# Kernel tuning notes

Hardware: AMD Instinct MI355X
Metric: run time of the kernel (lower is better)

## Reference

```python
import jax, jax.numpy as jnp
import numpy as np
from itertools import product

# dims
V, B, C, H, Wd = 3, 4, 64, 120, 160   # views, batch, feat2d_channel, image H/W
D3 = 96                               # feat3d_dim
G = 64                                # voxel grid side
N = 200000                            # sparse voxel count
NL = 250000                           # number of link rows
K = 27                                # 3^3 sparse-conv kernel offsets
EPS = 1e-5


def _build_kernel_map(rng):
    # unique sparse coordinates (b,x,y,z) sampled from a B*G^3 grid, sorted by linear code
    lin = np.sort(rng.choice(B * G * G * G, size=N, replace=False)).astype(np.int64)
    b = lin // (G * G * G)
    r = lin % (G * G * G)
    x = r // (G * G)
    y = (r // G) % G
    z = r % G
    in_idx = np.zeros((K, N), np.int32)
    mask = np.zeros((K, N), bool)
    for k, (dx, dy, dz) in enumerate(product((-1, 0, 1), repeat=3)):
        qx, qy, qz = x + dx, y + dy, z + dz
        inb = (qx >= 0) & (qx < G) & (qy >= 0) & (qy < G) & (qz >= 0) & (qz < G)
        qc = ((b * G + np.clip(qx, 0, G - 1)) * G + np.clip(qy, 0, G - 1)) * G + np.clip(qz, 0, G - 1)
        pos = np.clip(np.searchsorted(lin, qc), 0, N - 1)
        ok = inb & (lin[pos] == qc)
        in_idx[k] = np.where(ok, pos, 0)
        mask[k] = ok
    return jnp.asarray(in_idx), jnp.asarray(mask)


def setup_inputs() -> dict:
    rng = np.random.default_rng(0)
    key = jax.random.key(0)
    ks = jax.random.split(key, 8)
    feat_2d_all = jax.random.normal(ks[0], (V, B, C, H, Wd), jnp.float32)
    feat3d_F = jax.random.normal(ks[1], (N, D3), jnp.float32)
    # links: (NL, 4, V) = [batch_idx, v(row), u(col), valid]
    links = np.stack([
        rng.integers(0, B, (NL, V)),
        rng.integers(0, H, (NL, V)),
        rng.integers(0, Wd, (NL, V)),
        rng.integers(0, 2, (NL, V)),
    ], axis=1).astype(np.int32)
    coords_map_out = rng.permutation(N).astype(np.int32)
    coords_map_in = rng.choice(NL, N, replace=False).astype(np.int32)
    in_idx, nbr_mask = _build_kernel_map(rng)
    s = 0.05
    W1 = jax.random.normal(ks[2], (K, V * C, C), jnp.float32) * s
    W2 = jax.random.normal(ks[3], (K, C, D3), jnp.float32) * s
    W3 = jax.random.normal(ks[4], (K, 2 * D3, D3), jnp.float32) * s
    return {
        'feat_2d_all': feat_2d_all, 'feat3d_F': feat3d_F,
        'links': jnp.asarray(links),
        'coords_map_in': jnp.asarray(coords_map_in),
        'coords_map_out': jnp.asarray(coords_map_out),
        'in_idx': in_idx, 'nbr_mask': nbr_mask,
        'W1': W1, 'g1': jnp.ones((C,)), 'b1': jnp.zeros((C,)),
        'W2': W2, 'g2': jnp.ones((D3,)), 'b2': jnp.zeros((D3,)),
        'W3': W3, 'g3': jnp.ones((D3,)), 'b3': jnp.zeros((D3,)),
    }


def _sconv(x, Wk, in_idx, nbr_mask):
    # sparse 3x3x3 conv: out[i] = sum_k x[nbr(i,k)] @ Wk[k], masked where no neighbor
    out = jnp.zeros((x.shape[0], Wk.shape[-1]), x.dtype)
    for k in range(Wk.shape[0]):
        g = x[in_idx[k]] * nbr_mask[k][:, None].astype(x.dtype)
        out = out + g @ Wk[k]
    return out


def _bn_relu(x, g, b):
    mu = x.mean(axis=0)
    var = x.var(axis=0)
    return jax.nn.relu(g * (x - mu) / jnp.sqrt(var + EPS) + b)


def reference(feat_2d_all, feat3d_F, links, coords_map_in, coords_map_out,
              in_idx, nbr_mask, W1, g1, b1, W2, g2, b2, W3, g3, b3):
    n = feat3d_F.shape[0]
    v_, c = feat_2d_all.shape[0], feat_2d_all.shape[2]
    # current_links[coords_map_out] = links[coords_map_in]
    cur = jnp.zeros((n, 4, v_), links.dtype).at[coords_map_out].set(links[coords_map_in])
    bi = cur[:, 0, :].T   # (V, n)
    hi = cur[:, 1, :].T
    wi = cur[:, 2, :].T
    val = cur[:, 3, :].T
    vs = jnp.arange(v_)[:, None]
    # per-view gather from (V,B,C,H,W): advanced indices around the channel slice -> (V, n, C)
    g = feat_2d_all[vs, bi, :, hi, wi]
    g = g * val[:, :, None].astype(g.dtype)
    feat_2d_to_3d = jnp.transpose(g, (1, 0, 2)).reshape(n, v_ * c)
    # view_fusion: conv3 -> BN -> ReLU -> conv3 -> BN -> ReLU
    h = _bn_relu(_sconv(feat_2d_to_3d, W1, in_idx, nbr_mask), g1, b1)
    h = _bn_relu(_sconv(h, W2, in_idx, nbr_mask), g2, b2)
    # cat with 3d features, fuse_to_3d: conv3 -> BN -> ReLU
    cat = jnp.concatenate([feat3d_F, h], axis=-1)
    out = _bn_relu(_sconv(cat, W3, in_idx, nbr_mask), g3, b3)
    return out
```

## Files before the change

kernel.cpp:

```cpp
#include <hip/hip_runtime.h>
#include <stdint.h>


constexpr int NPT = 200000;
constexpr int KNB = 27;

typedef unsigned short u16;
typedef __attribute__((ext_vector_type(8))) short     bf16x8;
typedef __attribute__((ext_vector_type(8))) unsigned short u16x8;
typedef __attribute__((ext_vector_type(16))) float    f32x16;

static __device__ __forceinline__ u16 f2bf(float f){
  unsigned int u = __float_as_uint(f);
  unsigned int r = (u + 0x7fffu + ((u >> 16) & 1u)) >> 16;
  return (u16)r;
}
static __device__ __forceinline__ float bf2f(u16 u){
  return __uint_as_float(((unsigned int)u) << 16);
}

__global__ void detect_mask_kernel(const int* __restrict__ m32, int* __restrict__ flag){
  if (threadIdx.x == 0 && blockIdx.x == 0){
    int ok = 1;
    for (int i = 0; i < 64; ++i){ int v = m32[i]; if (v != 0 && v != 1) ok = 0; }
    *flag = ok;
  }
}

__global__ __launch_bounds__(256) void transpose2d_kernel(const float* __restrict__ in,
                                                          u16* __restrict__ out){
  __shared__ float tile[64][33];
  int bid = blockIdx.x;
  int wt = bid % 5;  int rest = bid / 5;
  int h  = rest % 120; rest /= 120;
  int b  = rest % 4;  int v = rest / 4;
  int w0 = wt * 32;
  int tx = threadIdx.x & 31;
  int ty = threadIdx.x >> 5;
  const float* ip = in + ((size_t)(v*4 + b) * 64) * 19200 + h * 160 + w0;
  #pragma unroll
  for (int cc = 0; cc < 8; ++cc){
    int c = cc * 8 + ty;
    tile[c][tx] = ip[(size_t)c * 19200 + tx];
  }
  __syncthreads();
  u16* op = out + (((size_t)(v*4 + b) * 120 + h) * 160 + w0) * 64;
  int c = threadIdx.x & 63;
  int wg = threadIdx.x >> 6;
  #pragma unroll
  for (int i = 0; i < 8; ++i){
    int w = wg + i * 4;
    op[(size_t)w * 64 + c] = f2bf(tile[c][w]);
  }
}

__global__ void wconvert_kernel(const float* __restrict__ src, u16* __restrict__ dst,
                                int cin, int cout){
  int gid = blockIdx.x * 256 + threadIdx.x;
  int wele = cin * cout;
  int tot = KNB * wele;
  if (gid >= tot) return;
  int ncb = cout / 32;
  int nks = cin / 16;
  int e    = gid & 7;
  int lane = (gid >> 3) & 63;
  int f    = gid >> 9;
  int cb   = f % ncb;  f /= ncb;
  int ks   = f % nks;
  int k    = f / nks;
  int ci = ks * 16 + (lane >> 5) * 8 + e;
  int co = cb * 32 + (lane & 31);
  dst[gid] = f2bf(src[((size_t)k * cin + ci) * cout + co]);
}

__global__ void stage_a_kernel(const u16* __restrict__ ft, const int* __restrict__ links,
                               const int* __restrict__ cmi, const int* __restrict__ cmo,
                               u16* __restrict__ x0){
  int gid = blockIdx.x * 256 + threadIdx.x;
  if (gid >= NPT * 3) return;
  int i = gid / 3;
  int v = gid - i * 3;
  int outr = cmo[i];
  int l    = cmi[i];
  int b  = links[l*12 + v];
  int h  = links[l*12 + 3 + v];
  int w  = links[l*12 + 6 + v];
  int vl = links[l*12 + 9 + v];
  u16* dst = x0 + (size_t)outr * 192 + v * 64;
  if (vl){
    const u16* src = ft + (((size_t)(v*4 + b) * 120 + h) * 160 + w) * 64;
    #pragma unroll
    for (int j = 0; j < 8; ++j) ((u16x8*)dst)[j] = ((const u16x8*)src)[j];
  } else {
    u16x8 z = {};
    #pragma unroll
    for (int j = 0; j < 8; ++j) ((u16x8*)dst)[j] = z;
  }
}

__global__ void f3convert_kernel(const float* __restrict__ src, u16* __restrict__ dst){
  long gid = (long)blockIdx.x * 256 + threadIdx.x;
  long tot8 = (long)NPT * 96 / 8;
  if (gid >= tot8) return;
  long e = gid * 8;
  #pragma unroll
  for (int j = 0; j < 8; ++j) dst[e + j] = f2bf(src[e + j]);
}

template<int CIN, int COUT, bool CONCAT, bool F32OUT>
__global__ __launch_bounds__(256)
void conv_kernel(const u16* __restrict__ x0, const u16* __restrict__ x1,
                 const u16* __restrict__ wt, const int* __restrict__ in_idx,
                 const uint8_t* __restrict__ mu8, const int* __restrict__ mi32,
                 const int* __restrict__ flagp, void* __restrict__ outp,
                 float* __restrict__ st){
  constexpr int NCB  = COUT / 32;
  constexpr int NKS  = CIN / 16;
  constexpr int WELE = CIN * COUT;
  constexpr int SEGS = WELE / 2048;
  __shared__ __align__(16) u16 wlds[WELE];
  __shared__ float shS[COUT], shQ[COUT];

  const int tid   = threadIdx.x;
  const int lane  = tid & 63;
  const int wv    = tid >> 6;
  const int l31   = lane & 31;
  const int khalf = lane >> 5;
  const int m0    = blockIdx.x * 256;
  const int fInt  = *flagp;

  f32x16 acc[2][NCB];
  #pragma unroll
  for (int rt = 0; rt < 2; ++rt)
    #pragma unroll
    for (int cb = 0; cb < NCB; ++cb) acc[rt][cb] = (f32x16)0.0f;

  u16x8 wpre[SEGS];
  #pragma unroll
  for (int s = 0; s < SEGS; ++s) wpre[s] = *(const u16x8*)&wt[tid*8 + s*2048];
  #pragma unroll
  for (int s = 0; s < SEGS; ++s) *(u16x8*)&wlds[tid*8 + s*2048] = wpre[s];
  __syncthreads();

  for (int k = 0; k < KNB; ++k){
    if (k + 1 < KNB){
      const u16* wn = wt + (size_t)(k+1) * WELE;
      #pragma unroll
      for (int s = 0; s < SEGS; ++s) wpre[s] = *(const u16x8*)&wn[tid*8 + s*2048];
    }

    int ids[2]; bool val[2];
    #pragma unroll
    for (int rt = 0; rt < 2; ++rt){
      int row  = m0 + wv * 64 + rt * 32 + l31;
      int rowc = row < NPT ? row : NPT - 1;
      ids[rt] = in_idx[k * NPT + rowc];
      int mv;
      if (fInt) mv = mi32[k * NPT + rowc];
      else      mv = (int)mu8[k * NPT + rowc];
      val[rt] = (mv != 0);
    }

    #pragma unroll
    for (int ks = 0; ks < NKS; ++ks){
      const int ci0 = ks * 16 + khalf * 8;
      bf16x8 a[2];
      #pragma unroll
      for (int rt = 0; rt < 2; ++rt){
        const u16* ap;
        if (CONCAT) ap = (ci0 < 96) ? (x0 + (size_t)ids[rt] * 96 + ci0)
                                    : (x1 + (size_t)ids[rt] * 96 + (ci0 - 96));
        else        ap = x0 + (size_t)ids[rt] * CIN + ci0;
        bf16x8 z = {};
        a[rt] = val[rt] ? *(const bf16x8*)ap : z;
      }
      #pragma unroll
      for (int cb = 0; cb < NCB; ++cb){
        bf16x8 b = *(const bf16x8*)&wlds[(ks * NCB + cb) * 512 + lane * 8];
        acc[0][cb] = __builtin_amdgcn_mfma_f32_32x32x16_bf16(a[0], b, acc[0][cb], 0, 0, 0);
        acc[1][cb] = __builtin_amdgcn_mfma_f32_32x32x16_bf16(a[1], b, acc[1][cb], 0, 0, 0);
      }
    }
    __syncthreads();
    if (k + 1 < KNB){
      #pragma unroll
      for (int s = 0; s < SEGS; ++s) *(u16x8*)&wlds[tid*8 + s*2048] = wpre[s];
      __syncthreads();
    }
  }

  if (tid < COUT){ shS[tid] = 0.f; shQ[tid] = 0.f; }
  __syncthreads();

  #pragma unroll
  for (int rt = 0; rt < 2; ++rt){
    #pragma unroll
    for (int cb = 0; cb < NCB; ++cb){
      const int cout = cb * 32 + l31;
      float s = 0.f, q = 0.f;
      #pragma unroll
      for (int r = 0; r < 16; ++r){
        int row = m0 + wv * 64 + rt * 32 + (r & 3) + 8 * (r >> 2) + 4 * khalf;
        if (row < NPT){
          float v = acc[rt][cb][r];
          if (F32OUT) ((float*)outp)[(size_t)row * COUT + cout] = v;
          else        ((u16*)outp)[(size_t)row * COUT + cout] = f2bf(v);
          s += v; q += v * v;
        }
      }
      atomicAdd(&shS[cout], s); atomicAdd(&shQ[cout], q);
    }
  }
  __syncthreads();
  if (tid < COUT){
    atomicAdd(&st[tid],        shS[tid]);
    atomicAdd(&st[COUT + tid], shQ[tid]);
  }
}

template<int CCH, bool ISF32>
__global__ void bnrelu_kernel(void* __restrict__ xp, const float* __restrict__ st,
                              const float* __restrict__ gg, const float* __restrict__ bb){
  const float invN = 1.0f / (float)NPT;
  long tot8 = (long)NPT * CCH / 8;
  for (long e8 = (long)blockIdx.x * 256 + threadIdx.x; e8 < tot8; e8 += (long)gridDim.x * 256){
    long e = e8 * 8;
    int c0 = (int)(e % CCH);
    #pragma unroll
    for (int j = 0; j < 8; ++j){
      int c = c0 + j;
      float mu  = st[c] * invN;
      float var = st[CCH + c] * invN - mu * mu;
      float rs  = rsqrtf(var + 1e-5f);
      float x;
      if (ISF32) x = ((float*)xp)[e + j];
      else       x = bf2f(((u16*)xp)[e + j]);
      float y = gg[c] * (x - mu) * rs + bb[c];
      y = y > 0.f ? y : 0.f;
      if (ISF32) ((float*)xp)[e + j] = y;
      else       ((u16*)xp)[e + j] = f2bf(y);
    }
  }
}

extern "C" void kernel_launch(void* const* d_in, const int* in_sizes, int n_in,
                              void* d_out, int out_size, void* d_ws, size_t ws_size,
                              hipStream_t stream){
  const float* feat2d = (const float*)d_in[0];
  const float* feat3d = (const float*)d_in[1];
  const int*   links  = (const int*)d_in[2];
  const int*   cmi    = (const int*)d_in[3];
  const int*   cmo    = (const int*)d_in[4];
  const int*   inidx  = (const int*)d_in[5];
  const void*  mask   = d_in[6];
  const float* W1 = (const float*)d_in[7];
  const float* g1 = (const float*)d_in[8];
  const float* b1 = (const float*)d_in[9];
  const float* W2 = (const float*)d_in[10];
  const float* g2 = (const float*)d_in[11];
  const float* b2 = (const float*)d_in[12];
  const float* W3 = (const float*)d_in[13];
  const float* g3 = (const float*)d_in[14];
  const float* b3 = (const float*)d_in[15];

  char* ws = (char*)d_ws;
  u16* X0 = (u16*)(ws + 0);
  u16* ZA = (u16*)(ws + 0);
  u16* F3 = (u16*)(ws + 38400000);
  u16* Z1 = (u16*)(ws + 76800000);
  u16* FT = (u16*)(ws + 76800000);
  u16* WT1 = (u16*)(ws + 106291200);
  u16* WT2 = WT1 + 27 * 192 * 64;
  u16* WT3 = WT2 + 27 * 64 * 96;
  float* ST  = (float*)(ws + 108281856);
  float* ST1 = ST;
  float* ST2 = ST + 128;
  float* ST3 = ST + 320;
  int*   FLAG = (int*)(ST + 512);

  hipMemsetAsync(ST, 0, 513 * sizeof(float), stream);
  detect_mask_kernel<<<1, 64, 0, stream>>>((const int*)mask, FLAG);
  transpose2d_kernel<<<7200, 256, 0, stream>>>(feat2d, FT);
  wconvert_kernel<<<(27*192*64 + 255)/256, 256, 0, stream>>>(W1, WT1, 192, 64);
  wconvert_kernel<<<(27*64*96  + 255)/256, 256, 0, stream>>>(W2, WT2, 64, 96);
  wconvert_kernel<<<(27*192*96 + 255)/256, 256, 0, stream>>>(W3, WT3, 192, 96);
  stage_a_kernel<<<(NPT*3 + 255)/256, 256, 0, stream>>>(FT, links, cmi, cmo, X0);

  const int nblk = (NPT + 255) / 256;
  const uint8_t* m8 = (const uint8_t*)mask;
  const int* m32 = (const int*)mask;

  conv_kernel<192, 64, false, false><<<nblk, 256, 0, stream>>>(X0, nullptr, WT1, inidx, m8, m32, FLAG, Z1, ST1);
  bnrelu_kernel<64, false><<<2048, 256, 0, stream>>>(Z1, ST1, g1, b1);

  f3convert_kernel<<<((NPT*96/8) + 255)/256, 256, 0, stream>>>(feat3d, F3);

  conv_kernel<64, 96, false, false><<<nblk, 256, 0, stream>>>(Z1, nullptr, WT2, inidx, m8, m32, FLAG, ZA, ST2);
  bnrelu_kernel<96, false><<<2048, 256, 0, stream>>>(ZA, ST2, g2, b2);

  conv_kernel<192, 96, true, true><<<nblk, 256, 0, stream>>>(F3, ZA, WT3, inidx, m8, m32, FLAG, d_out, ST3);
  bnrelu_kernel<96, true><<<2048, 256, 0, stream>>>(d_out, ST3, g3, b3);
}
```

Before: 923.1 us.

## Switch sparse conv to 16x16x32 MFMA with double-buffered weights and column split

```diff
diff --git a/kernel.cpp b/kernel.cpp
--- a/kernel.cpp
+++ b/kernel.cpp
@@ -8,7 +8,7 @@
 typedef unsigned short u16;
 typedef __attribute__((ext_vector_type(8))) short     bf16x8;
 typedef __attribute__((ext_vector_type(8))) unsigned short u16x8;
-typedef __attribute__((ext_vector_type(16))) float    f32x16;
+typedef __attribute__((ext_vector_type(4))) float     f32x4;
 
 static __device__ __forceinline__ u16 f2bf(float f){
   unsigned int u = __float_as_uint(f);
@@ -55,22 +55,21 @@
 }
 
 __global__ void wconvert_kernel(const float* __restrict__ src, u16* __restrict__ dst,
-                                int cin, int cout){
+                                int cin, int coutT, int coutF, int cbase){
   int gid = blockIdx.x * 256 + threadIdx.x;
-  int wele = cin * cout;
-  int tot = KNB * wele;
+  int tot = KNB * cin * coutT;
   if (gid >= tot) return;
-  int ncb = cout / 32;
-  int nks = cin / 16;
+  int ncb = coutT / 16;
+  int nkc = cin / 32;
   int e    = gid & 7;
   int lane = (gid >> 3) & 63;
   int f    = gid >> 9;
   int cb   = f % ncb;  f /= ncb;
-  int ks   = f % nks;
-  int k    = f / nks;
-  int ci = ks * 16 + (lane >> 5) * 8 + e;
-  int co = cb * 32 + (lane & 31);
-  dst[gid] = f2bf(src[((size_t)k * cin + ci) * cout + co]);
+  int kc   = f % nkc;
+  int k    = f / nkc;
+  int ci = kc * 32 + (lane >> 4) * 8 + e;
+  int co = cbase + cb * 16 + (lane & 15);
+  dst[gid] = f2bf(src[((size_t)k * cin + ci) * coutF + co]);
 }
 
 __global__ void stage_a_kernel(const u16* __restrict__ ft, const int* __restrict__ links,
@@ -107,104 +106,139 @@
   for (int j = 0; j < 8; ++j) dst[e + j] = f2bf(src[e + j]);
 }
 
-template<int CIN, int COUT, bool CONCAT, bool F32OUT>
+template<int CIN, int COUT_T, bool CONCAT, bool COLSPLIT, bool F32OUT>
 __global__ __launch_bounds__(256)
 void conv_kernel(const u16* __restrict__ x0, const u16* __restrict__ x1,
-                 const u16* __restrict__ wt, const int* __restrict__ in_idx,
+                 const u16* __restrict__ wtA, const u16* __restrict__ wtB,
+                 const int* __restrict__ in_idx,
                  const uint8_t* __restrict__ mu8, const int* __restrict__ mi32,
                  const int* __restrict__ flagp, void* __restrict__ outp,
                  float* __restrict__ st){
-  constexpr int NCB  = COUT / 32;
-  constexpr int NKS  = CIN / 16;
-  constexpr int WELE = CIN * COUT;
-  constexpr int SEGS = WELE / 2048;
-  __shared__ __align__(16) u16 wlds[WELE];
-  __shared__ float shS[COUT], shQ[COUT];
+  constexpr int NCB   = COUT_T / 16;
+  constexpr int NKC   = CIN / 32;
+  constexpr int WELE  = CIN * COUT_T;
+  constexpr int SEGS  = (WELE + 2047) / 2048;
+  constexpr int COUTF = COLSPLIT ? COUT_T * 2 : COUT_T;
+  __shared__ __align__(16) u16 wlds[2 * WELE];
+  __shared__ float shS[COUT_T], shQ[COUT_T];
 
   const int tid   = threadIdx.x;
   const int lane  = tid & 63;
   const int wv    = tid >> 6;
-  const int l31   = lane & 31;
-  const int khalf = lane >> 5;
-  const int m0    = blockIdx.x * 256;
+  const int r16   = lane & 15;
+  const int kgrp  = lane >> 4;
+  const int bid   = blockIdx.x;
+  const int half  = COLSPLIT ? (bid & 1) : 0;
+  const int m0    = (COLSPLIT ? (bid >> 1) : bid) * 128;
+  const int cbase = half * COUT_T;
+  const u16* wt   = (COLSPLIT && half) ? wtB : wtA;
   const int fInt  = *flagp;
 
-  f32x16 acc[2][NCB];
+  if (tid < COUT_T){ shS[tid] = 0.f; shQ[tid] = 0.f; }
+
+  f32x4 acc[2][NCB];
   #pragma unroll
   for (int rt = 0; rt < 2; ++rt)
     #pragma unroll
-    for (int cb = 0; cb < NCB; ++cb) acc[rt][cb] = (f32x16)0.0f;
-
-  u16x8 wpre[SEGS];
-  #pragma unroll
-  for (int s = 0; s < SEGS; ++s) wpre[s] = *(const u16x8*)&wt[tid*8 + s*2048];
-  #pragma unroll
-  for (int s = 0; s < SEGS; ++s) *(u16x8*)&wlds[tid*8 + s*2048] = wpre[s];
+    for (int cb = 0; cb < NCB; ++cb) acc[rt][cb] = (f32x4)0.0f;
+
+  int rowc[2];
+  #pragma unroll
+  for (int rt = 0; rt < 2; ++rt){
+    int row = m0 + wv * 32 + rt * 16 + r16;
+    rowc[rt] = row < NPT ? row : NPT - 1;
+  }
+
+  #pragma unroll
+  for (int s = 0; s < SEGS; ++s){
+    int off = (tid + s * 256) * 8;
+    if (off < WELE) *(u16x8*)&wlds[off] = *(const u16x8*)&wt[off];
+  }
+  int idC[2]; bool mC[2];
+  #pragma unroll
+  for (int rt = 0; rt < 2; ++rt){
+    idC[rt] = in_idx[rowc[rt]];
+    int mv = fInt ? mi32[rowc[rt]] : (int)mu8[rowc[rt]];
+    mC[rt] = (mv != 0);
+  }
   __syncthreads();
 
   for (int k = 0; k < KNB; ++k){
+    u16x8 wpre[SEGS];
     if (k + 1 < KNB){
-      const u16* wn = wt + (size_t)(k+1) * WELE;
-      #pragma unroll
-      for (int s = 0; s < SEGS; ++s) wpre[s] = *(const u16x8*)&wn[tid*8 + s*2048];
-    }
-
-    int ids[2]; bool val[2];
+      const u16* wn = wt + (size_t)(k + 1) * WELE;
+      #pragma unroll
+      for (int s = 0; s < SEGS; ++s){
+        int off = (tid + s * 256) * 8;
+        if (off < WELE) wpre[s] = *(const u16x8*)&wn[off];
+      }
+    }
+    int idN[2]; bool mN[2];
+    if (k + 1 < KNB){
+      #pragma unroll
+      for (int rt = 0; rt < 2; ++rt){
+        idN[rt] = in_idx[(k + 1) * NPT + rowc[rt]];
+        int mv = fInt ? mi32[(k + 1) * NPT + rowc[rt]] : (int)mu8[(k + 1) * NPT + rowc[rt]];
+        mN[rt] = (mv != 0);
+      }
+    }
+
+    bf16x8 a[2][NKC];
     #pragma unroll
     for (int rt = 0; rt < 2; ++rt){
-      int row  = m0 + wv * 64 + rt * 32 + l31;
-      int rowc = row < NPT ? row : NPT - 1;
-      ids[rt] = in_idx[k * NPT + rowc];
-      int mv;
-      if (fInt) mv = mi32[k * NPT + rowc];
-      else      mv = (int)mu8[k * NPT + rowc];
-      val[rt] = (mv != 0);
-    }
-
-    #pragma unroll
-    for (int ks = 0; ks < NKS; ++ks){
-      const int ci0 = ks * 16 + khalf * 8;
-      bf16x8 a[2];
-      #pragma unroll
-      for (int rt = 0; rt < 2; ++rt){
-        const u16* ap;
-        if (CONCAT) ap = (ci0 < 96) ? (x0 + (size_t)ids[rt] * 96 + ci0)
-                                    : (x1 + (size_t)ids[rt] * 96 + (ci0 - 96));
-        else        ap = x0 + (size_t)ids[rt] * CIN + ci0;
-        bf16x8 z = {};
-        a[rt] = val[rt] ? *(const bf16x8*)ap : z;
-      }
+      if (mC[rt]){
+        #pragma unroll
+        for (int kc = 0; kc < NKC; ++kc){
+          int ci0 = kc * 32 + kgrp * 8;
+          const u16* ap;
+          if (CONCAT) ap = (ci0 < 96) ? (x0 + (size_t)idC[rt] * 96 + ci0)
+                                      : (x1 + (size_t)idC[rt] * 96 + (ci0 - 96));
+          else        ap = x0 + (size_t)idC[rt] * CIN + ci0;
+          a[rt][kc] = *(const bf16x8*)ap;
+        }
+      } else {
+        #pragma unroll
+        for (int kc = 0; kc < NKC; ++kc){ bf16x8 z = {}; a[rt][kc] = z; }
+      }
+    }
+
+    const u16* wb = &wlds[(k & 1) * WELE];
+    #pragma unroll
+    for (int kc = 0; kc < NKC; ++kc){
       #pragma unroll
       for (int cb = 0; cb < NCB; ++cb){
-        bf16x8 b = *(const bf16x8*)&wlds[(ks * NCB + cb) * 512 + lane * 8];
-        acc[0][cb] = __builtin_amdgcn_mfma_f32_32x32x16_bf16(a[0], b, acc[0][cb], 0, 0, 0);
-        acc[1][cb] = __builtin_amdgcn_mfma_f32_32x32x16_bf16(a[1], b, acc[1][cb], 0, 0, 0);
-      }
+        bf16x8 b = *(const bf16x8*)&wb[((kc * NCB + cb) * 64 + lane) * 8];
+        acc[0][cb] = __builtin_amdgcn_mfma_f32_16x16x32_bf16(a[0][kc], b, acc[0][cb], 0, 0, 0);
+        acc[1][cb] = __builtin_amdgcn_mfma_f32_16x16x32_bf16(a[1][kc], b, acc[1][cb], 0, 0, 0);
+      }
+    }
+
+    if (k + 1 < KNB){
+      u16* wd = &wlds[((k + 1) & 1) * WELE];
+      #pragma unroll
+      for (int s = 0; s < SEGS; ++s){
+        int off = (tid + s * 256) * 8;
+        if (off < WELE) *(u16x8*)&wd[off] = wpre[s];
+      }
+      #pragma unroll
+      for (int rt = 0; rt < 2; ++rt){ idC[rt] = idN[rt]; mC[rt] = mN[rt]; }
     }
     __syncthreads();
-    if (k + 1 < KNB){
-      #pragma unroll
-      for (int s = 0; s < SEGS; ++s) *(u16x8*)&wlds[tid*8 + s*2048] = wpre[s];
-      __syncthreads();
-    }
-  }
-
-  if (tid < COUT){ shS[tid] = 0.f; shQ[tid] = 0.f; }
-  __syncthreads();
+  }
 
   #pragma unroll
   for (int rt = 0; rt < 2; ++rt){
     #pragma unroll
     for (int cb = 0; cb < NCB; ++cb){
-      const int cout = cb * 32 + l31;
+      const int cout = cb * 16 + r16;
       float s = 0.f, q = 0.f;
       #pragma unroll
-      for (int r = 0; r < 16; ++r){
-        int row = m0 + wv * 64 + rt * 32 + (r & 3) + 8 * (r >> 2) + 4 * khalf;
+      for (int j = 0; j < 4; ++j){
+        int row = m0 + wv * 32 + rt * 16 + kgrp * 4 + j;
         if (row < NPT){
-          float v = acc[rt][cb][r];
-          if (F32OUT) ((float*)outp)[(size_t)row * COUT + cout] = v;
-          else        ((u16*)outp)[(size_t)row * COUT + cout] = f2bf(v);
+          float v = acc[rt][cb][j];
+          if (F32OUT) ((float*)outp)[(size_t)row * COUTF + cbase + cout] = v;
+          else        ((u16*)outp)[(size_t)row * COUTF + cbase + cout] = f2bf(v);
           s += v; q += v * v;
         }
       }
@@ -212,9 +246,9 @@
     }
   }
   __syncthreads();
-  if (tid < COUT){
-    atomicAdd(&st[tid],        shS[tid]);
-    atomicAdd(&st[COUT + tid], shQ[tid]);
+  if (tid < COUT_T){
+    atomicAdd(&st[cbase + tid],         shS[tid]);
+    atomicAdd(&st[COUTF + cbase + tid], shQ[tid]);
   }
 }
 
@@ -269,9 +303,10 @@
   u16* F3 = (u16*)(ws + 38400000);
   u16* Z1 = (u16*)(ws + 76800000);
   u16* FT = (u16*)(ws + 76800000);
-  u16* WT1 = (u16*)(ws + 106291200);
-  u16* WT2 = WT1 + 27 * 192 * 64;
-  u16* WT3 = WT2 + 27 * 64 * 96;
+  u16* WT1  = (u16*)(ws + 106291200);
+  u16* WT2  = WT1 + 27 * 192 * 64;
+  u16* WT3a = WT2 + 27 * 64 * 96;
+  u16* WT3b = WT3a + 27 * 192 * 48;
   float* ST  = (float*)(ws + 108281856);
   float* ST1 = ST;
   float* ST2 = ST + 128;
@@ -281,23 +316,24 @@
   hipMemsetAsync(ST, 0, 513 * sizeof(float), stream);
   detect_mask_kernel<<<1, 64, 0, stream>>>((const int*)mask, FLAG);
   transpose2d_kernel<<<7200, 256, 0, stream>>>(feat2d, FT);
-  wconvert_kernel<<<(27*192*64 + 255)/256, 256, 0, stream>>>(W1, WT1, 192, 64);
-  wconvert_kernel<<<(27*64*96  + 255)/256, 256, 0, stream>>>(W2, WT2, 64, 96);
-  wconvert_kernel<<<(27*192*96 + 255)/256, 256, 0, stream>>>(W3, WT3, 192, 96);
+  wconvert_kernel<<<(27*192*64 + 255)/256, 256, 0, stream>>>(W1, WT1, 192, 64, 64, 0);
+  wconvert_kernel<<<(27*64*96  + 255)/256, 256, 0, stream>>>(W2, WT2, 64, 96, 96, 0);
+  wconvert_kernel<<<(27*192*48 + 255)/256, 256, 0, stream>>>(W3, WT3a, 192, 48, 96, 0);
+  wconvert_kernel<<<(27*192*48 + 255)/256, 256, 0, stream>>>(W3, WT3b, 192, 48, 96, 48);
   stage_a_kernel<<<(NPT*3 + 255)/256, 256, 0, stream>>>(FT, links, cmi, cmo, X0);
 
-  const int nblk = (NPT + 255) / 256;
+  const int nblk = (NPT + 127) / 128;
   const uint8_t* m8 = (const uint8_t*)mask;
   const int* m32 = (const int*)mask;
 
-  conv_kernel<192, 64, false, false><<<nblk, 256, 0, stream>>>(X0, nullptr, WT1, inidx, m8, m32, FLAG, Z1, ST1);
+  conv_kernel<192, 64, false, false, false><<<nblk, 256, 0, stream>>>(X0, nullptr, WT1, nullptr, inidx, m8, m32, FLAG, Z1, ST1);
   bnrelu_kernel<64, false><<<2048, 256, 0, stream>>>(Z1, ST1, g1, b1);
 
   f3convert_kernel<<<((NPT*96/8) + 255)/256, 256, 0, stream>>>(feat3d, F3);
 
-  conv_kernel<64, 96, false, false><<<nblk, 256, 0, stream>>>(Z1, nullptr, WT2, inidx, m8, m32, FLAG, ZA, ST2);
+  conv_kernel<64, 96, false, false, false><<<nblk, 256, 0, stream>>>(Z1, nullptr, WT2, nullptr, inidx, m8, m32, FLAG, ZA, ST2);
   bnrelu_kernel<96, false><<<2048, 256, 0, stream>>>(ZA, ST2, g2, b2);
 
-  conv_kernel<192, 96, true, true><<<nblk, 256, 0, stream>>>(F3, ZA, WT3, inidx, m8, m32, FLAG, d_out, ST3);
+  conv_kernel<192, 48, true, true, true><<<2 * nblk, 256, 0, stream>>>(F3, ZA, WT3a, WT3b, inidx, m8, m32, FLAG, d_out, ST3);
   bnrelu_kernel<96, true><<<2048, 256, 0, stream>>>(d_out, ST3, g3, b3);
 }
```

Result: faster. 896.1 us (-2.9%).

## Use direct-to-LDS weight loads, zero-row masking, and interleaved concat buffer

Applied to the files above, without the earlier changes.

```diff
diff --git a/kernel.cpp b/kernel.cpp
--- a/kernel.cpp
+++ b/kernel.cpp
@@ -17,6 +17,13 @@
 }
 static __device__ __forceinline__ float bf2f(u16 u){
   return __uint_as_float(((unsigned int)u) << 16);
+}
+
+static __device__ __forceinline__ void gload_lds16(const void* g, void* l){
+  __builtin_amdgcn_global_load_lds(
+      (const __attribute__((address_space(1))) void*)g,
+      (__attribute__((address_space(3))) void*)(uint32_t)(uintptr_t)l,
+      16, 0, 0);
 }
 
 __global__ void detect_mask_kernel(const int* __restrict__ m32, int* __restrict__ flag){
@@ -100,24 +107,27 @@
 
 __global__ void f3convert_kernel(const float* __restrict__ src, u16* __restrict__ dst){
   long gid = (long)blockIdx.x * 256 + threadIdx.x;
-  long tot8 = (long)NPT * 96 / 8;
+  long tot8 = (long)NPT * 12;
   if (gid >= tot8) return;
-  long e = gid * 8;
-  #pragma unroll
-  for (int j = 0; j < 8; ++j) dst[e + j] = f2bf(src[e + j]);
-}
-
-template<int CIN, int COUT, bool CONCAT, bool F32OUT>
+  int row = (int)(gid / 12);
+  int c0  = (int)(gid % 12) * 8;
+  const float* s = src + (size_t)row * 96 + c0;
+  u16* d = dst + (size_t)row * 192 + c0;
+  #pragma unroll
+  for (int j = 0; j < 8; ++j) d[j] = f2bf(s[j]);
+}
+
+template<int CIN, int COUT, bool F32OUT>
 __global__ __launch_bounds__(256)
-void conv_kernel(const u16* __restrict__ x0, const u16* __restrict__ x1,
-                 const u16* __restrict__ wt, const int* __restrict__ in_idx,
+void conv_kernel(const u16* __restrict__ x0, const u16* __restrict__ wt,
+                 const int* __restrict__ in_idx,
                  const uint8_t* __restrict__ mu8, const int* __restrict__ mi32,
                  const int* __restrict__ flagp, void* __restrict__ outp,
-                 float* __restrict__ st){
-  constexpr int NCB  = COUT / 32;
-  constexpr int NKS  = CIN / 16;
-  constexpr int WELE = CIN * COUT;
-  constexpr int SEGS = WELE / 2048;
+                 int outStride, float* __restrict__ st){
+  constexpr int NCB    = COUT / 32;
+  constexpr int NKC    = CIN / 16;
+  constexpr int WELE   = CIN * COUT;
+  constexpr int ROUNDS = (WELE * 2) / 4096;
   __shared__ __align__(16) u16 wlds[WELE];
   __shared__ float shS[COUT], shQ[COUT];
 
@@ -129,68 +139,76 @@
   const int m0    = blockIdx.x * 256;
   const int fInt  = *flagp;
 
+  if (tid < COUT){ shS[tid] = 0.f; shQ[tid] = 0.f; }
+
   f32x16 acc[2][NCB];
   #pragma unroll
   for (int rt = 0; rt < 2; ++rt)
     #pragma unroll
     for (int cb = 0; cb < NCB; ++cb) acc[rt][cb] = (f32x16)0.0f;
 
-  u16x8 wpre[SEGS];
-  #pragma unroll
-  for (int s = 0; s < SEGS; ++s) wpre[s] = *(const u16x8*)&wt[tid*8 + s*2048];
-  #pragma unroll
-  for (int s = 0; s < SEGS; ++s) *(u16x8*)&wlds[tid*8 + s*2048] = wpre[s];
+  int rowc[2];
+  #pragma unroll
+  for (int rt = 0; rt < 2; ++rt){
+    int row = m0 + wv * 64 + rt * 32 + l31;
+    rowc[rt] = row < NPT ? row : NPT - 1;
+  }
+
+  #pragma unroll
+  for (int rd = 0; rd < ROUNDS; ++rd){
+    int chunk = rd * 4 + wv;
+    gload_lds16((const char*)wt + chunk * 1024 + lane * 16,
+                (char*)wlds + chunk * 1024);
+  }
+  int vC[2];
+  #pragma unroll
+  for (int rt = 0; rt < 2; ++rt){
+    int id = in_idx[rowc[rt]];
+    int mv; if (fInt) mv = mi32[rowc[rt]]; else mv = (int)mu8[rowc[rt]];
+    vC[rt] = mv ? id : NPT;
+  }
   __syncthreads();
 
+  const u16* xk = x0 + khalf * 8;
+
   for (int k = 0; k < KNB; ++k){
+    const u16* b0 = xk + (size_t)vC[0] * CIN;
+    const u16* b1 = xk + (size_t)vC[1] * CIN;
+
     if (k + 1 < KNB){
-      const u16* wn = wt + (size_t)(k+1) * WELE;
-      #pragma unroll
-      for (int s = 0; s < SEGS; ++s) wpre[s] = *(const u16x8*)&wn[tid*8 + s*2048];
-    }
-
-    int ids[2]; bool val[2];
-    #pragma unroll
-    for (int rt = 0; rt < 2; ++rt){
-      int row  = m0 + wv * 64 + rt * 32 + l31;
-      int rowc = row < NPT ? row : NPT - 1;
-      ids[rt] = in_idx[k * NPT + rowc];
-      int mv;
-      if (fInt) mv = mi32[k * NPT + rowc];
-      else      mv = (int)mu8[k * NPT + rowc];
-      val[rt] = (mv != 0);
-    }
-
-    #pragma unroll
-    for (int ks = 0; ks < NKS; ++ks){
-      const int ci0 = ks * 16 + khalf * 8;
-      bf16x8 a[2];
       #pragma unroll
       for (int rt = 0; rt < 2; ++rt){
-        const u16* ap;
-        if (CONCAT) ap = (ci0 < 96) ? (x0 + (size_t)ids[rt] * 96 + ci0)
-                                    : (x1 + (size_t)ids[rt] * 96 + (ci0 - 96));
-        else        ap = x0 + (size_t)ids[rt] * CIN + ci0;
-        bf16x8 z = {};
-        a[rt] = val[rt] ? *(const bf16x8*)ap : z;
+        int o = (k + 1) * NPT + rowc[rt];
+        int id = in_idx[o];
+        int mv; if (fInt) mv = mi32[o]; else mv = (int)mu8[o];
+        vC[rt] = mv ? id : NPT;
       }
+    }
+
+    #pragma unroll
+    for (int kc = 0; kc < NKC; ++kc){
+      bf16x8 a0 = *(const bf16x8*)(b0 + kc * 16);
+      bf16x8 a1 = *(const bf16x8*)(b1 + kc * 16);
       #pragma unroll
       for (int cb = 0; cb < NCB; ++cb){
-        bf16x8 b = *(const bf16x8*)&wlds[(ks * NCB + cb) * 512 + lane * 8];
-        acc[0][cb] = __builtin_amdgcn_mfma_f32_32x32x16_bf16(a[0], b, acc[0][cb], 0, 0, 0);
-        acc[1][cb] = __builtin_amdgcn_mfma_f32_32x32x16_bf16(a[1], b, acc[1][cb], 0, 0, 0);
+        bf16x8 b = *(const bf16x8*)&wlds[((kc * NCB + cb) * 64 + lane) * 8];
+        acc[0][cb] = __builtin_amdgcn_mfma_f32_32x32x16_bf16(a0, b, acc[0][cb], 0, 0, 0);
+        acc[1][cb] = __builtin_amdgcn_mfma_f32_32x32x16_bf16(a1, b, acc[1][cb], 0, 0, 0);
       }
     }
     __syncthreads();
+
     if (k + 1 < KNB){
+      const u16* wn = wt + (size_t)(k + 1) * WELE;
       #pragma unroll
-      for (int s = 0; s < SEGS; ++s) *(u16x8*)&wlds[tid*8 + s*2048] = wpre[s];
-      __syncthreads();
-    }
-  }
-
-  if (tid < COUT){ shS[tid] = 0.f; shQ[tid] = 0.f; }
-  __syncthreads();
+      for (int rd = 0; rd < ROUNDS; ++rd){
+        int chunk = rd * 4 + wv;
+        gload_lds16((const char*)wn + chunk * 1024 + lane * 16,
+                    (char*)wlds + chunk * 1024);
+      }
+    }
+    __syncthreads();
+  }
 
   #pragma unroll
   for (int rt = 0; rt < 2; ++rt){
@@ -203,8 +221,8 @@
         int row = m0 + wv * 64 + rt * 32 + (r & 3) + 8 * (r >> 2) + 4 * khalf;
         if (row < NPT){
           float v = acc[rt][cb][r];
-          if (F32OUT) ((float*)outp)[(size_t)row * COUT + cout] = v;
-          else        ((u16*)outp)[(size_t)row * COUT + cout] = f2bf(v);
+          if (F32OUT) ((float*)outp)[(size_t)row * outStride + cout] = v;
+          else        ((u16*)outp)[(size_t)row * outStride + cout] = f2bf(v);
           s += v; q += v * v;
         }
       }
@@ -219,13 +237,16 @@
 }
 
 template<int CCH, bool ISF32>
-__global__ void bnrelu_kernel(void* __restrict__ xp, const float* __restrict__ st,
+__global__ void bnrelu_kernel(void* __restrict__ xp, int stride,
+                              const float* __restrict__ st,
                               const float* __restrict__ gg, const float* __restrict__ bb){
   const float invN = 1.0f / (float)NPT;
-  long tot8 = (long)NPT * CCH / 8;
+  constexpr int GPR = CCH / 8;
+  long tot8 = (long)NPT * GPR;
   for (long e8 = (long)blockIdx.x * 256 + threadIdx.x; e8 < tot8; e8 += (long)gridDim.x * 256){
-    long e = e8 * 8;
-    int c0 = (int)(e % CCH);
+    int row = (int)(e8 / GPR);
+    int c0  = (int)(e8 % GPR) * 8;
+    size_t base = (size_t)row * stride + c0;
     #pragma unroll
     for (int j = 0; j < 8; ++j){
       int c = c0 + j;
@@ -233,12 +254,12 @@
       float var = st[CCH + c] * invN - mu * mu;
       float rs  = rsqrtf(var + 1e-5f);
       float x;
-      if (ISF32) x = ((float*)xp)[e + j];
-      else       x = bf2f(((u16*)xp)[e + j]);
+      if (ISF32) x = ((float*)xp)[base + j];
+      else       x = bf2f(((u16*)xp)[base + j]);
       float y = gg[c] * (x - mu) * rs + bb[c];
       y = y > 0.f ? y : 0.f;
-      if (ISF32) ((float*)xp)[e + j] = y;
-      else       ((u16*)xp)[e + j] = f2bf(y);
+      if (ISF32) ((float*)xp)[base + j] = y;
+      else       ((u16*)xp)[base + j] = f2bf(y);
     }
   }
 }
@@ -265,14 +286,13 @@
 
   char* ws = (char*)d_ws;
   u16* X0 = (u16*)(ws + 0);
-  u16* ZA = (u16*)(ws + 0);
-  u16* F3 = (u16*)(ws + 38400000);
-  u16* Z1 = (u16*)(ws + 76800000);
-  u16* FT = (u16*)(ws + 76800000);
-  u16* WT1 = (u16*)(ws + 106291200);
+  constexpr size_t OFF_B  = 76800512;
+  u16* FT = (u16*)(ws + OFF_B);
+  u16* Z1 = (u16*)(ws + OFF_B);
+  u16* WT1 = (u16*)(ws + 106291712);
   u16* WT2 = WT1 + 27 * 192 * 64;
   u16* WT3 = WT2 + 27 * 64 * 96;
-  float* ST  = (float*)(ws + 108281856);
+  float* ST  = (float*)(ws + 108282368);
   float* ST1 = ST;
   float* ST2 = ST + 128;
   float* ST3 = ST + 320;
@@ -286,18 +306,21 @@
   wconvert_kernel<<<(27*192*96 + 255)/256, 256, 0, stream>>>(W3, WT3, 192, 96);
   stage_a_kernel<<<(NPT*3 + 255)/256, 256, 0, stream>>>(FT, links, cmi, cmo, X0);
 
+  hipMemsetAsync(ws + (size_t)NPT * 384, 0, 384, stream);
+  hipMemsetAsync(ws + OFF_B + (size_t)NPT * 128, 0, 128, stream);
+
   const int nblk = (NPT + 255) / 256;
   const uint8_t* m8 = (const uint8_t*)mask;
   const int* m32 = (const int*)mask;
 
-  conv_kernel<192, 64, false, false><<<nblk, 256, 0, stream>>>(X0, nullptr, WT1, inidx, m8, m32, FLAG, Z1, ST1);
-  bnrelu_kernel<64, false><<<2048, 256, 0, stream>>>(Z1, ST1, g1, b1);
-
-  f3convert_kernel<<<((NPT*96/8) + 255)/256, 256, 0, stream>>>(feat3d, F3);
-
-  conv_kernel<64, 96, false, false><<<nblk, 256, 0, stream>>>(Z1, nullptr, WT2, inidx, m8, m32, FLAG, ZA, ST2);
-  bnrelu_kernel<96, false><<<2048, 256, 0, stream>>>(ZA, ST2, g2, b2);
-
-  conv_kernel<192, 96, true, true><<<nblk, 256, 0, stream>>>(F3, ZA, WT3, inidx, m8, m32, FLAG, d_out, ST3);
-  bnrelu_kernel<96, true><<<2048, 256, 0, stream>>>(d_out, ST3, g3, b3);
-}
+  conv_kernel<192, 64, false><<<nblk, 256, 0, stream>>>(X0, WT1, inidx, m8, m32, FLAG, Z1, 64, ST1);
+  bnrelu_kernel<64, false><<<2048, 256, 0, stream>>>(Z1, 64, ST1, g1, b1);
+
+  f3convert_kernel<<<((NPT*12) + 255)/256, 256, 0, stream>>>(feat3d, X0);
+
+  conv_kernel<64, 96, false><<<nblk, 256, 0, stream>>>(Z1, WT2, inidx, m8, m32, FLAG, X0 + 96, 192, ST2);
+  bnrelu_kernel<96, false><<<2048, 256, 0, stream>>>(X0 + 96, 192, ST2, g2, b2);
+
+  conv_kernel<192, 96, true><<<nblk, 256, 0, stream>>>(X0, WT3, inidx, m8, m32, FLAG, d_out, 96, ST3);
+  bnrelu_kernel<96, true><<<2048, 256, 0, stream>>>(d_out, 96, ST3, g3, b3);
+}
```

Measured after the change: 763.3 us. -17.3%, faster.
